# Optimization experiments

Measured on AMD Instinct MI355X. Metric: run time of the kernel, lower is better.

The kernel has to match this reference:

```python
import jax, jax.numpy as jnp
import numpy as np

B, CIN, COUT = 4, 32, 32
D1, D2, D3 = 64, 64, 64
M1, M2, M3 = 32, 32, 17  # n_modes with last dim -> 32//2+1 after rfft redundancy
INIT_STD = (2.0 / (CIN + COUT)) ** 0.5


def setup_inputs() -> dict:
    key = jax.random.key(0)
    k_x, k_wr, k_wi, k_b = jax.random.split(key, 4)
    x = jax.random.normal(k_x, (B, CIN, D1, D2, D3), dtype=jnp.float32)
    # ComplexDense factorized weight, normal_(0, init_std) on real and imag parts
    w_real = INIT_STD * jax.random.normal(k_wr, (CIN, COUT, M1, M2, M3), dtype=jnp.float32)
    w_imag = INIT_STD * jax.random.normal(k_wi, (CIN, COUT, M1, M2, M3), dtype=jnp.float32)
    # bias: (n_layers=1, out_channels, 1, 1, 1); we take index 0 slice
    bias = INIT_STD * jax.random.normal(k_b, (1, COUT, 1, 1, 1), dtype=jnp.float32)
    return {"x": x, "w_real": w_real, "w_imag": w_imag, "bias": bias}


def reference(x, w_real, w_imag, bias):
    fft_axes = (-3, -2, -1)
    b, cin, d1, d2, d3 = x.shape
    f3 = d3 // 2 + 1
    # forward rFFT, shift all but last (real) axis so low modes are centered
    xf = jnp.fft.rfftn(x, axes=fft_axes)               # (B, Cin, D1, D2, f3) complex
    xf = jnp.fft.fftshift(xf, axes=fft_axes[:-1])
    weight = w_real + 1j * w_imag                       # (Cin, Cout, M1, M2, M3)
    m1, m2, m3 = weight.shape[2:]
    s1, s2 = (d1 - m1) // 2, (d2 - m2) // 2
    xs = xf[:, :, s1:s1 + m1, s2:s2 + m2, :m3]          # centered low modes
    # channel contraction in Fourier space: abcde,bfcde->afcde
    out_modes = jnp.einsum('abcde,bfcde->afcde', xs, weight)
    out_fft = jnp.zeros((b, weight.shape[1], d1, d2, f3), dtype=out_modes.dtype)
    out_fft = out_fft.at[:, :, s1:s1 + m1, s2:s2 + m2, :m3].set(out_modes)
    # torch applies fftshift (not ifftshift); identical for even sizes
    out_fft = jnp.fft.fftshift(out_fft, axes=fft_axes[:-1])
    out = jnp.fft.irfftn(out_fft, s=(d1, d2, d3), axes=fft_axes)
    return out + bias[0]
```

## Files before the change

kernel.cpp:

```cpp
#include <hip/hip_runtime.h>
#include <math.h>

static constexpr int NB  = 4;
static constexpr int NC  = 32;

__device__ __attribute__((aligned(256))) float T3F[64 * 48];
__device__ __attribute__((aligned(256))) float2 T3I2[17 * 64];
__device__ __attribute__((aligned(256))) float T12F[64 * 64];
__device__ __attribute__((aligned(256))) float TINV[32 * 128];

__global__ __launch_bounds__(256) void k0_init() {
    const int t = blockIdx.x * 256 + threadIdx.x;
    if (t < 64 * 17) {
        int n = t / 17, k = t % 17;
        int idx = (n * k) & 63;
        float s, c;
        sincospif(idx / 32.0f, &s, &c);
        T3F[n * 48 + 2 * k] = c;  T3F[n * 48 + 2 * k + 1] = -s;
    }
    if (t < 64) {
        for (int q = 34; q < 48; ++q) T3F[t * 48 + q] = 0.f;
    }
    if (t < 17 * 64) {
        int k = t >> 6, n = t & 63;
        int idx = (n * k) & 63;
        float s, c;
        sincospif(idx / 32.0f, &s, &c);
        T3I2[t] = make_float2(c, s);
    }
    if (t < 64 * 32) {
        int n = t / 32, p = t % 32;
        int o = (p + 48) & 63;
        int idx = (o * n) & 63;
        float s, c;
        sincospif(idx / 32.0f, &s, &c);
        T12F[n * 64 + 2 * p] = c;  T12F[n * 64 + 2 * p + 1] = -s;
    }
    if (t < 32 * 64) {
        int p = t / 64, n = t % 64;
        int o = (p + 48) & 63;
        int idx = (o * n) & 63;
        float s, c;
        sincospif(idx / 32.0f, &s, &c);
        TINV[p * 128 + 2 * n] = c;  TINV[p * 128 + 2 * n + 1] = s;
    }
}

__device__ __forceinline__ void cmadd(float2& a, float2 x, float wx, float wy) {
    a.x = fmaf(x.x, wx, fmaf(-x.y, wy, a.x));
    a.y = fmaf(x.x, wy, fmaf( x.y, wx, a.y));
}

__global__ __launch_bounds__(64)
void k12_rfft_dft(const float* __restrict__ x, float2* __restrict__ T) {
    __shared__ __align__(16) float smem[64 * 65];
    float* tile = smem;
    float2* XE = (float2*)smem;
    float2* XO = XE + 17 * 33;
    const int t = threadIdx.x, bid = blockIdx.x;
    const float4* src4 = (const float4*)(x + (size_t)bid * 4096);
    for (int j = 0; j < 16; ++j) {
        int f4 = j * 64 + t;
        float4 v = src4[f4];
        int d2 = f4 >> 4, n0 = (f4 & 15) << 2;
        float* p = &tile[d2 * 65 + n0];
        p[0] = v.x; p[1] = v.y; p[2] = v.z; p[3] = v.w;
    }
    float ar[17], ai[17];
#pragma unroll
    for (int k = 0; k < 17; ++k) { ar[k] = 0.f; ai[k] = 0.f; }
    const float* row = &tile[t * 65];
    for (int n = 0; n < 32; ++n) {
        float xa = row[n], xb = row[n + 32];
        float se = xa + xb, so = xa - xb;
        const float* w = &T3F[n * 48];
#pragma unroll
        for (int k = 0; k < 17; ++k) {
            float xv = (k & 1) ? so : se;
            ar[k] = fmaf(xv, w[2 * k], ar[k]);
            ai[k] = fmaf(xv, w[2 * k + 1], ai[k]);
        }
    }
    const int lane = t;
    const int nl = lane & 31;
#pragma unroll
    for (int k = 0; k < 17; ++k) {
        float pr = __shfl_xor(ar[k], 32);
        float pi = __shfl_xor(ai[k], 32);
        if (lane < 32) XE[k * 33 + nl] = make_float2(ar[k] + pr, ai[k] + pi);
        else           XO[k * 33 + nl] = make_float2(pr - ar[k], pi - ai[k]);
    }
    const int p2 = lane & 31;
    const int kh = lane >> 5;
    float2 twv[32];
#pragma unroll
    for (int n = 0; n < 32; ++n)
        twv[n] = *(const float2*)&T12F[n * 64 + 2 * p2];
    const float2* Xs = (p2 & 1) ? XO : XE;
    const int bc = bid >> 6, d1 = bid & 63;
#pragma unroll
    for (int j = 0; j < 9; ++j) {
        int k3 = kh * 9 + j;
        if (k3 < 17) {
            float2 s = make_float2(0.f, 0.f);
            const float2* xr = &Xs[k3 * 33];
#pragma unroll
            for (int n2 = 0; n2 < 32; ++n2)
                cmadd(s, xr[n2], twv[n2].x, twv[n2].y);
            T[((size_t)bc * 17 + k3) * 2048 + d1 * 32 + p2] = s;
        }
    }
}

__global__ __launch_bounds__(544)
void k2b_dft_d1(const float2* __restrict__ T, float2* __restrict__ Y) {
    __shared__ float2 tile[8 * 544];
    const int u = threadIdx.x;
    const int bc = blockIdx.x, pg = blockIdx.y;
    const int k3 = u >> 5, p2 = u & 31;
    const float2* src = T + ((size_t)bc * 17 + k3) * 2048 + p2;
    float2 acc[8];
#pragma unroll
    for (int j = 0; j < 8; ++j) acc[j] = make_float2(0.f, 0.f);
#pragma unroll 2
    for (int n1 = 0; n1 < 64; ++n1) {
        float2 xv = src[n1 * 32];
        const float* w = &T12F[n1 * 64 + pg * 16];
#pragma unroll
        for (int j = 0; j < 8; ++j)
            cmadd(acc[j], xv, w[2 * j], w[2 * j + 1]);
    }
#pragma unroll
    for (int j = 0; j < 8; ++j)
        tile[j * 544 + p2 * 17 + k3] = acc[j];
    __syncthreads();
    float2* dst = Y + (size_t)bc * 17408 + (size_t)pg * 8 * 544;
#pragma unroll
    for (int i = 0; i < 8; ++i)
        dst[u + i * 544] = tile[u + i * 544];
}

__global__ __launch_bounds__(64)
void k3_mix(const float2* __restrict__ Y, const float* __restrict__ wr,
            const float* __restrict__ wi, float2* __restrict__ Z) {
    const int m = blockIdx.x * 64 + threadIdx.x;
    const int ch = blockIdx.y;
    float2 acc[4][2];
#pragma unroll
    for (int a = 0; a < 4; ++a)
#pragma unroll
        for (int co = 0; co < 2; ++co) acc[a][co] = make_float2(0.f, 0.f);
#pragma unroll 8
    for (int cin = 0; cin < 32; ++cin) {
        float2 xv[4];
#pragma unroll
        for (int a = 0; a < 4; ++a)
            xv[a] = Y[((size_t)a * 32 + cin) * 17408 + m];
        size_t wb = ((size_t)cin * 32 + ch * 2) * 17408 + m;
#pragma unroll
        for (int co = 0; co < 2; ++co) {
            float wrv = wr[wb + (size_t)co * 17408];
            float wiv = wi[wb + (size_t)co * 17408];
#pragma unroll
            for (int a = 0; a < 4; ++a)
                cmadd(acc[a][co], xv[a], wrv, wiv);
        }
    }
#pragma unroll
    for (int a = 0; a < 4; ++a)
#pragma unroll
        for (int co = 0; co < 2; ++co)
            Z[((size_t)a * 32 + ch * 2 + co) * 17408 + m] = acc[a][co];
}

__global__ __launch_bounds__(544)
void k4a_idft_d1(const float2* __restrict__ Z, float2* __restrict__ U) {
    const int u = threadIdx.x;
    const int bf = blockIdx.x, ng = blockIdx.y;
    const float2* src = Z + (size_t)bf * 17408 + u;
    float2 acc[8];
#pragma unroll
    for (int j = 0; j < 8; ++j) acc[j] = make_float2(0.f, 0.f);
#pragma unroll 2
    for (int p1 = 0; p1 < 32; ++p1) {
        float2 xv = src[(size_t)p1 * 544];
        const float* w = &TINV[p1 * 128 + ng * 16];
#pragma unroll
        for (int j = 0; j < 8; ++j)
            cmadd(acc[j], xv, w[2 * j], w[2 * j + 1]);
    }
    float2* dst = U + (size_t)bf * 34816 + (size_t)ng * 8 * 544 + u;
#pragma unroll
    for (int j = 0; j < 8; ++j) dst[(size_t)j * 544] = acc[j];
}

__global__ __launch_bounds__(256)
void k45_ifft23(const float2* __restrict__ U, const float* __restrict__ bias,
                float* __restrict__ out) {
    __shared__ __align__(16) float2 Ur[32 * 18];
    __shared__ float2 W2[17 * 64];
    const int t = threadIdx.x;
    const int bf = blockIdx.x, n1 = blockIdx.y;
    const float2* src = U + (size_t)bf * 34816 + (size_t)n1 * 544;
    for (int j = t; j < 544; j += 256) {
        int p2 = j / 17, k3 = j - p2 * 17;
        Ur[p2 * 18 + k3] = src[j];
    }
    const int lane = t & 63;
    const int w = __builtin_amdgcn_readfirstlane(t >> 6);
    float2 tws[32];
#pragma unroll
    for (int p = 0; p < 32; ++p)
        tws[p] = *(const float2*)&TINV[p * 128 + 2 * lane];
    __syncthreads();
    const float inv2 = 2.0f / 262144.0f;
    {
        const int kb = w * 4;
        float A[4] = {0,0,0,0}, Bm[4] = {0,0,0,0};
        float C[4] = {0,0,0,0}, Dm[4] = {0,0,0,0};
#pragma unroll
        for (int p2 = 0; p2 < 32; ++p2) {
            float4 xa = *(const float4*)&Ur[p2 * 18 + kb];
            float4 xb = *(const float4*)&Ur[p2 * 18 + kb + 2];
            float c = tws[p2].x, s = tws[p2].y;
            A[0] = fmaf(xa.x, c, A[0]);  Bm[0] = fmaf(xa.y, s, Bm[0]);
            C[0] = fmaf(xa.x, s, C[0]);  Dm[0] = fmaf(xa.y, c, Dm[0]);
            A[1] = fmaf(xa.z, c, A[1]);  Bm[1] = fmaf(xa.w, s, Bm[1]);
            C[1] = fmaf(xa.z, s, C[1]);  Dm[1] = fmaf(xa.w, c, Dm[1]);
            A[2] = fmaf(xb.x, c, A[2]);  Bm[2] = fmaf(xb.y, s, Bm[2]);
            C[2] = fmaf(xb.x, s, C[2]);  Dm[2] = fmaf(xb.y, c, Dm[2]);
            A[3] = fmaf(xb.z, c, A[3]);  Bm[3] = fmaf(xb.w, s, Bm[3]);
            C[3] = fmaf(xb.z, s, C[3]);  Dm[3] = fmaf(xb.w, c, Dm[3]);
        }
#pragma unroll
        for (int j = 0; j < 4; ++j)
            W2[(kb + j) * 64 + lane] =
                make_float2((A[j] - Bm[j]) * inv2, (C[j] + Dm[j]) * inv2);
        if (w == 3) {
            float a = 0.f, b = 0.f, c2 = 0.f, d = 0.f;
#pragma unroll
            for (int p2 = 0; p2 < 32; ++p2) {
                float2 xv = Ur[p2 * 18 + 16];
                float c = tws[p2].x, s = tws[p2].y;
                a  = fmaf(xv.x, c, a);   b = fmaf(xv.y, s, b);
                c2 = fmaf(xv.x, s, c2);  d = fmaf(xv.y, c, d);
            }
            W2[16 * 64 + lane] = make_float2((a - b) * inv2, (c2 + d) * inv2);
        }
    }
    __syncthreads();
    float2 X[17];
#pragma unroll
    for (int k = 0; k < 17; ++k) X[k] = W2[k * 64 + lane];
    const float bv = bias[bf & 31];
    float y[16];
#pragma unroll
    for (int r = 0; r < 16; ++r) y[r] = fmaf(X[0].x, 0.5f, bv);
#pragma unroll
    for (int k = 1; k < 17; ++k) {
        const float2* tr = &T3I2[k * 64 + w * 16];
#pragma unroll
        for (int r = 0; r < 16; ++r) {
            float2 tw = tr[r];
            y[r] = fmaf(X[k].x, tw.x, y[r]);
            y[r] = fmaf(-X[k].y, tw.y, y[r]);
        }
    }
    float* dst = out + (size_t)bf * 262144 + (size_t)n1 * 4096
               + (size_t)lane * 64 + w * 16;
#pragma unroll
    for (int q = 0; q < 4; ++q)
        *(float4*)&dst[q * 4] =
            make_float4(y[q * 4], y[q * 4 + 1], y[q * 4 + 2], y[q * 4 + 3]);
}

extern "C" void kernel_launch(void* const* d_in, const int* in_sizes, int n_in,
                              void* d_out, int out_size, void* d_ws, size_t ws_size,
                              hipStream_t stream) {
    const float* x    = (const float*)d_in[0];
    const float* wr   = (const float*)d_in[1];
    const float* wi   = (const float*)d_in[2];
    const float* bias = (const float*)d_in[3];
    float* out = (float*)d_out;

    float2* A = (float2*)d_ws;
    float2* B = A + (size_t)2176 * 4096;
    float2* Y = A;
    float2* Z = A + (size_t)17825792 / 8;

    k0_init     <<<8, 256, 0, stream>>>();
    k12_rfft_dft<<<NB * NC * 64, 64, 0, stream>>>(x, B);
    k2b_dft_d1  <<<dim3(128, 4), 544, 0, stream>>>(B, Y);
    k3_mix      <<<dim3(272, 16), 64, 0, stream>>>(Y, wr, wi, Z);
    k4a_idft_d1 <<<dim3(128, 8), 544, 0, stream>>>(Z, B);
    k45_ifft23  <<<dim3(128, 64), 256, 0, stream>>>(B, bias, out);
}
```

Measured before the change: 247.6 us.

## Fuse inverse d1 DFT into the d2/d3 inverse FFT kernel

Removes the separate k4a_idft_d1 kernel and its intermediate U buffer. Each (bf, n1) block of the final kernel now computes its own row of the inverse d1 DFT straight from Z into shared memory. This saves one launch and a write plus reread of the intermediate. The cost is that every n1 block rereads the full 32x544 Z slab for its bf, so Z is read 64 times from cache/global instead of once per 8-output group.

```diff
diff --git a/kernel.cpp b/kernel.cpp
--- a/kernel.cpp
+++ b/kernel.cpp
@@ -173,45 +173,49 @@
             Z[((size_t)a * 32 + ch * 2 + co) * 17408 + m] = acc[a][co];
 }
 
-__global__ __launch_bounds__(544)
-void k4a_idft_d1(const float2* __restrict__ Z, float2* __restrict__ U) {
-    const int u = threadIdx.x;
-    const int bf = blockIdx.x, ng = blockIdx.y;
-    const float2* src = Z + (size_t)bf * 17408 + u;
-    float2 acc[8];
-#pragma unroll
-    for (int j = 0; j < 8; ++j) acc[j] = make_float2(0.f, 0.f);
-#pragma unroll 2
-    for (int p1 = 0; p1 < 32; ++p1) {
-        float2 xv = src[(size_t)p1 * 544];
-        const float* w = &TINV[p1 * 128 + ng * 16];
-#pragma unroll
-        for (int j = 0; j < 8; ++j)
-            cmadd(acc[j], xv, w[2 * j], w[2 * j + 1]);
-    }
-    float2* dst = U + (size_t)bf * 34816 + (size_t)ng * 8 * 544 + u;
-#pragma unroll
-    for (int j = 0; j < 8; ++j) dst[(size_t)j * 544] = acc[j];
-}
-
 __global__ __launch_bounds__(256)
-void k45_ifft23(const float2* __restrict__ U, const float* __restrict__ bias,
-                float* __restrict__ out) {
+void k45z_ifft123(const float2* __restrict__ Z, const float* __restrict__ bias,
+                  float* __restrict__ out) {
     __shared__ __align__(16) float2 Ur[32 * 18];
     __shared__ float2 W2[17 * 64];
     const int t = threadIdx.x;
     const int bf = blockIdx.x, n1 = blockIdx.y;
-    const float2* src = U + (size_t)bf * 34816 + (size_t)n1 * 544;
-    for (int j = t; j < 544; j += 256) {
-        int p2 = j / 17, k3 = j - p2 * 17;
-        Ur[p2 * 18 + k3] = src[j];
-    }
     const int lane = t & 63;
     const int w = __builtin_amdgcn_readfirstlane(t >> 6);
     float2 tws[32];
 #pragma unroll
     for (int p = 0; p < 32; ++p)
         tws[p] = *(const float2*)&TINV[p * 128 + 2 * lane];
+    {
+        const float2* zb = Z + (size_t)bf * 17408;
+        float2 a0 = make_float2(0.f, 0.f), a1 = a0, a2 = a0;
+#pragma unroll
+        for (int p1 = 0; p1 < 32; ++p1) {
+            const float c = TINV[p1 * 128 + 2 * n1];
+            const float s = TINV[p1 * 128 + 2 * n1 + 1];
+            const float2* zr = zb + p1 * 544;
+            float2 z0 = zr[t];
+            float2 z1 = zr[t + 256];
+            cmadd(a0, z0, c, s);
+            cmadd(a1, z1, c, s);
+            if (t < 32) {
+                float2 z2 = zr[t + 512];
+                cmadd(a2, z2, c, s);
+            }
+        }
+        {
+            int p2 = t / 17, k3 = t - p2 * 17;
+            Ur[p2 * 18 + k3] = a0;
+        }
+        {
+            int j = t + 256; int p2 = j / 17, k3 = j - p2 * 17;
+            Ur[p2 * 18 + k3] = a1;
+        }
+        if (t < 32) {
+            int j = t + 512; int p2 = j / 17, k3 = j - p2 * 17;
+            Ur[p2 * 18 + k3] = a2;
+        }
+    }
     __syncthreads();
     const float inv2 = 2.0f / 262144.0f;
     {
@@ -292,6 +296,5 @@
     k12_rfft_dft<<<NB * NC * 64, 64, 0, stream>>>(x, B);
     k2b_dft_d1  <<<dim3(128, 4), 544, 0, stream>>>(B, Y);
     k3_mix      <<<dim3(272, 16), 64, 0, stream>>>(Y, wr, wi, Z);
-    k4a_idft_d1 <<<dim3(128, 8), 544, 0, stream>>>(Z, B);
-    k45_ifft23  <<<dim3(128, 64), 256, 0, stream>>>(B, bias, out);
-}
+    k45z_ifft123<<<dim3(128, 64), 256, 0, stream>>>(Z, bias, out);
+}
```

Result: slower. 356.2 us (+43.9%).
